# Kernel tuning notes

Hardware: AMD Instinct MI355X
Metric: run time of the kernel (lower is better)

The kernel has to match this reference:

```python
import jax, jax.numpy as jnp
import numpy as np

WAY = 100; SHOT = 5; QUERY = 100; DIM = 2048; K_VALUE = 512
NQ = WAY * QUERY  # 10000 query samples


def _l2norm(x, axis=-1):
    n = jnp.linalg.norm(x, axis=axis, keepdims=True)
    return x / jnp.maximum(n, 1e-12)  # matches F.normalize eps


def _compute_logits(feat, proto, temp):
    # feat [1,Q,D], proto [1,W,D] -> [1,Q,W]; 'dot' metric
    logits = jnp.einsum('bqd,bwd->bqw', feat, proto)
    norm = jnp.linalg.norm(logits, axis=1, keepdims=True)  # L2 over query dim, [1,1,W]
    return logits / (norm + 1e-6) * temp


def _proto_refine(logits, feat, proto, k_value):
    # vectorized version of the original Python loop with .item() scatter-adds
    abs_cert = jnp.max(logits, axis=2)[0]                 # [Q]
    k = min(abs_cert.shape[0], k_value)
    vals, idxs = jax.lax.top_k(abs_cert, k)               # [k]
    pseudo = jnp.argmax(logits[0, idxs], axis=1)          # [k] pseudo labels
    wf = (vals[:, None] * feat[0, idxs]) / k              # [k,D]
    add = jnp.zeros(proto.shape[1:], feat.dtype).at[pseudo].add(wf)  # [W,D]
    return proto + add


def _distance(shot, feat, temp_proto, way):
    proto = _l2norm(jnp.mean(shot, axis=-2))  # [1,W,D]
    feat = _l2norm(feat)                      # [1,Q,D]
    logits = _compute_logits(feat, proto, temp_proto)
    proto = _proto_refine(logits, feat, proto, K_VALUE)
    logits = _compute_logits(feat, proto, temp_proto)
    return logits.reshape(-1, way)[None]      # [1,Q,W]


def _distill_loss(logits_l, logits_h, weight):
    # faithful to F.log_softmax/softmax over dim=1 (query dim) and the
    # per-batch-row weighted KL sum in the original
    logp = jax.nn.log_softmax(logits_l, axis=1)
    p = jax.nn.softmax(logits_h, axis=1)
    kl = p * (jnp.log(p) - logp)              # [B,Q,W]
    wT = weight.T                             # [Q,B]
    summed = jnp.stack([jnp.sum(kl[i] * wT[i]) for i in range(logits_l.shape[0])])
    return jnp.mean(summed) / (jnp.sum(weight) + 1e-8)


def _certainties(shot, query, temp_proto, way):
    pk = _distance(shot, query, temp_proto, way)
    abs_c = jnp.max(pk, axis=2)                           # [1,Q]
    p = jax.nn.softmax(pk, axis=-1)
    rel_c = jnp.sum(p * jnp.log(p + 1e-10), axis=2)       # [1,Q]
    return abs_c, rel_c


def setup_inputs() -> dict:
    key = jax.random.key(0)
    k1, k2, k3, k4 = jax.random.split(key, 4)
    return {
        'x_shot': jax.random.normal(k1, (1, WAY, SHOT, DIM), jnp.float32),
        'x_query': jax.random.normal(k2, (1, NQ, DIM), jnp.float32),
        'dct_shot': jax.random.normal(k3, (1, WAY, SHOT, DIM), jnp.float32),
        'dct_query': jax.random.normal(k4, (1, NQ, DIM), jnp.float32),
        'temp_proto': jnp.float32(10.0),
        'temp': jnp.float32(1.0),
        'temp_dct': jnp.float32(1.0),
    }


def reference(x_shot, x_query, dct_shot, dct_query, temp_proto, temp, temp_dct):
    way = x_shot.shape[1]
    abs_c, rel_c = _certainties(x_shot, x_query, temp_proto, way)
    abs_cd, rel_cd = _certainties(dct_shot, dct_query, temp_proto, way)
    diff = np.asarray(abs_c - abs_cd + rel_c - rel_cd)[0]
    res_idx = np.where(diff > 0)[0]
    dct_idx = np.where(diff < 0)[0]
    zero = jnp.float32(0.0)
    if res_idx.size == 0 and dct_idx.size == 0:
        loss_dctl = zero; loss_resl = zero
    elif res_idx.size != 0 and dct_idx.size == 0:
        lrh = _distance(x_shot, x_query, temp_proto, way)
        ldl = _distance(dct_shot, dct_query, temp_proto, way)
        loss_dctl = _distill_loss(ldl, lrh, abs_c); loss_resl = zero
    elif res_idx.size == 0:
        ldh = _distance(dct_shot, dct_query, temp_proto, way)
        lrl = _distance(x_shot, x_query, temp_proto, way)
        loss_resl = _distill_loss(lrl, ldh, abs_cd); loss_dctl = zero
    else:
        lrh = _distance(x_shot, x_query[:, res_idx], temp_proto, way)
        ldl = _distance(dct_shot, dct_query[:, res_idx], temp_proto, way)
        ldh = _distance(dct_shot, dct_query[:, dct_idx], temp_proto, way)
        lrl = _distance(x_shot, x_query[:, dct_idx], temp_proto, way)
        loss_dctl = _distill_loss(ldl, lrh, abs_c[:, res_idx])
        loss_resl = _distill_loss(lrl, ldh, abs_cd[:, dct_idx])
    denom = jnp.maximum(abs_c + abs_cd, 1e-8)
    w_r = (abs_c / denom).T  # [Q,1]
    w_f = (abs_cd / denom).T
    return (temp * loss_resl, temp_dct * loss_dctl,
            jnp.asarray(res_idx), jnp.asarray(dct_idx), w_r, w_f)
```

## Files before the change

kernel.cpp:

```cpp
#include <hip/hip_runtime.h>
#include <cstdint>
#include <cstddef>

#define WAYS  100
#define SHOTS 5
#define NQ    10000
#define DIM   2048
#define KSEL  512

#define BQ 64
#define BW 64
#define BK 32
#define PAD 4
#define CQ 64

struct Ctrl {
  double klsum[2];
  double wsum[2];
  float  w0[2];
  int    R, Dn;
  unsigned int T[8];
  int rem[8];
  int kk[8];
};

__device__ __forceinline__ unsigned int monokey(float f){
  unsigned int b = __float_as_uint(f);
  return (b & 0x80000000u) ? ~b : (b | 0x80000000u);
}
__device__ __forceinline__ float dekey(unsigned int k){
  return (k & 0x80000000u) ? __uint_as_float(k & 0x7FFFFFFFu)
                           : __uint_as_float(~k);
}
__device__ __forceinline__ int decn(int sel, const Ctrl* c){
  return sel == 0 ? NQ : (sel == 1 ? c->R : c->Dn);
}

__global__ void proto_kernel(const float* __restrict__ xs, const float* __restrict__ dsh,
                             float* __restrict__ protoX, float* __restrict__ protoD){
  int b = blockIdx.x;
  const float* src = (b < WAYS) ? xs : dsh;
  float* dst = (b < WAYS) ? protoX : protoD;
  int w = (b < WAYS) ? b : b - WAYS;
  __shared__ float meanv[DIM];
  __shared__ float red[256];
  float loc = 0.f;
  for (int d = threadIdx.x; d < DIM; d += 256){
    float s = 0.f;
    for (int sh = 0; sh < SHOTS; sh++) s += src[((size_t)w*SHOTS + sh)*DIM + d];
    float m = s / (float)SHOTS;
    meanv[d] = m;
    loc += m*m;
  }
  red[threadIdx.x] = loc; __syncthreads();
  for (int st = 128; st > 0; st >>= 1){
    if (threadIdx.x < st) red[threadIdx.x] += red[threadIdx.x + st];
    __syncthreads();
  }
  float inv = 1.0f / fmaxf(sqrtf(red[0]), 1e-12f);
  for (int d = threadIdx.x; d < DIM; d += 256)
    dst[(size_t)w*DIM + d] = meanv[d] * inv;
}

__global__ __launch_bounds__(256)
void invnorm_kernel(const float* __restrict__ xq, const float* __restrict__ dq,
                    float* __restrict__ invnX, float* __restrict__ invnD){
  int row = blockIdx.x * 4 + (threadIdx.x >> 6);
  if (row >= 2*NQ) return;
  int lane = threadIdx.x & 63;
  const float* src = (row < NQ) ? xq : dq;
  float* dst = (row < NQ) ? invnX : invnD;
  int q = (row < NQ) ? row : row - NQ;
  const float4* r4 = (const float4*)(src + (size_t)q*DIM);
  float s = 0.f;
  for (int i = lane; i < DIM/4; i += 64){
    float4 v = r4[i];
    s += v.x*v.x + v.y*v.y + v.z*v.z + v.w*v.w;
  }
  for (int off = 32; off > 0; off >>= 1) s += __shfl_down(s, off);
  if (lane == 0) dst[q] = 1.0f / fmaxf(sqrtf(s), 1e-12f);
}

struct GemmArgs {
  const float* feat[4];
  const float* proto[4];
  const int*   idx[4];
  float*       outP[4];
  const float* invn[4];
  int          nSel[4];
  int          offSel[4];
  int          splitk;
  int          applyInvn;
  const Ctrl*  ctrl;
};

__global__ __launch_bounds__(256)
void gemm_batched(GemmArgs ga){
  int batch = blockIdx.z / ga.splitk;
  int s     = blockIdx.z % ga.splitk;
  int n = decn(ga.nSel[batch], ga.ctrl);
  int qBase = blockIdx.x * BQ;
  if (qBase >= n) return;
  int wBase = blockIdx.y * BW;
  int kLen  = DIM / ga.splitk;
  int kStart = s * kLen;

  __shared__ float As[BK][BQ+PAD];
  __shared__ float Bs[BK][BW+PAD];

  const float* feat  = ga.feat[batch];
  const float* proto = ga.proto[batch];
  const int*   idxl  = ga.idx[batch];

  int t = threadIdx.x;
  int lr = t & 63;
  int kv = t >> 6;
  int arow = qBase + lr;
  int garow = idxl ? idxl[min(arow, n-1)] : min(arow, n-1);
  const float* pA = feat + (size_t)garow*DIM + kStart + kv*4;
  int wrow = wBase + lr;
  bool bok = (wrow < WAYS);
  const float* pB = proto + (size_t)wrow*DIM + kStart + kv*4;

  int tx = t & 15, ty = t >> 4;
  float acc[4][4];
#pragma unroll
  for (int i = 0; i < 4; i++)
#pragma unroll
    for (int j = 0; j < 4; j++) acc[i][j] = 0.f;

  float4 av0, av1, bv0, bv1;
  const float4 z4 = make_float4(0.f,0.f,0.f,0.f);
  av0 = *(const float4*)pA;
  av1 = *(const float4*)(pA + 16);
  bv0 = bok ? *(const float4*)pB : z4;
  bv1 = bok ? *(const float4*)(pB + 16) : z4;

  for (int k0 = 0; k0 < kLen; k0 += BK){
    __syncthreads();
    int kk = kv*4;
    As[kk+0 ][lr]=av0.x; As[kk+1 ][lr]=av0.y; As[kk+2 ][lr]=av0.z; As[kk+3 ][lr]=av0.w;
    As[kk+16][lr]=av1.x; As[kk+17][lr]=av1.y; As[kk+18][lr]=av1.z; As[kk+19][lr]=av1.w;
    Bs[kk+0 ][lr]=bv0.x; Bs[kk+1 ][lr]=bv0.y; Bs[kk+2 ][lr]=bv0.z; Bs[kk+3 ][lr]=bv0.w;
    Bs[kk+16][lr]=bv1.x; Bs[kk+17][lr]=bv1.y; Bs[kk+18][lr]=bv1.z; Bs[kk+19][lr]=bv1.w;
    __syncthreads();
    if (k0 + BK < kLen){
      const float* qA = pA + k0 + BK;
      const float* qB = pB + k0 + BK;
      av0 = *(const float4*)qA; av1 = *(const float4*)(qA + 16);
      bv0 = bok ? *(const float4*)qB : z4;
      bv1 = bok ? *(const float4*)(qB + 16) : z4;
    }
#pragma unroll
    for (int kk2 = 0; kk2 < BK; kk2++){
      float4 a = *(const float4*)&As[kk2][ty*4];
      float4 b = *(const float4*)&Bs[kk2][tx*4];
      acc[0][0]+=a.x*b.x; acc[0][1]+=a.x*b.y; acc[0][2]+=a.x*b.z; acc[0][3]+=a.x*b.w;
      acc[1][0]+=a.y*b.x; acc[1][1]+=a.y*b.y; acc[1][2]+=a.y*b.z; acc[1][3]+=a.y*b.w;
      acc[2][0]+=a.z*b.x; acc[2][1]+=a.z*b.y; acc[2][2]+=a.z*b.z; acc[2][3]+=a.z*b.w;
      acc[3][0]+=a.w*b.x; acc[3][1]+=a.w*b.y; acc[3][2]+=a.w*b.z; acc[3][3]+=a.w*b.w;
    }
  }
  int rowOff = ga.offSel[batch] ? ga.ctrl->R : 0;
  float* outBase = ga.outP[batch] + ((size_t)s*NQ + (size_t)rowOff)*WAYS;
  int wc = wBase + tx*4;
#pragma unroll
  for (int i = 0; i < 4; i++){
    int q = qBase + ty*4 + i;
    if (q >= n) continue;
    float scr = 1.f;
    if (ga.applyInvn){
      int gq = idxl ? idxl[q] : q;
      scr = ga.invn[batch][gq];
    }
    float* dst = outBase + (size_t)q*WAYS + wc;
    if (wc + 3 < WAYS){
      *(float4*)dst = make_float4(acc[i][0]*scr, acc[i][1]*scr, acc[i][2]*scr, acc[i][3]*scr);
    } else {
#pragma unroll
      for (int j = 0; j < 4; j++) if (wc + j < WAYS) dst[j] = acc[i][j]*scr;
    }
  }
}

struct CombArgs {
  const float* P;
  const float* invn[2];
  float* Ltgt[2];
  double* colSq;
  int splitk;
};
__global__ __launch_bounds__(256)
void combine_batched(CombArgs ca){
  int b = blockIdx.y;
  int qBase = blockIdx.x * CQ;
  int t = threadIdx.x;
  int j = t % 25, r = t / 25;
  const float* Pb = ca.P + (size_t)b*ca.splitk*NQ*WAYS;
  const float* invn = ca.invn[b];
  float* L = ca.Ltgt[b];
  double sq0=0.0, sq1=0.0, sq2=0.0, sq3=0.0;
  if (r < 10){
    for (int i = r; i < CQ; i += 10){
      int q = qBase + i;
      if (q >= NQ) break;
      float sc = invn[q];
      const float* p0 = Pb + (size_t)q*WAYS + 4*j;
      float4 v = *(const float4*)p0;
      for (int s2 = 1; s2 < ca.splitk; s2++){
        float4 u = *(const float4*)(p0 + (size_t)s2*NQ*WAYS);
        v.x += u.x; v.y += u.y; v.z += u.z; v.w += u.w;
      }
      v.x *= sc; v.y *= sc; v.z *= sc; v.w *= sc;
      *(float4*)(L + (size_t)q*WAYS + 4*j) = v;
      sq0 += (double)v.x*(double)v.x;
      sq1 += (double)v.y*(double)v.y;
      sq2 += (double)v.z*(double)v.z;
      sq3 += (double)v.w*(double)v.w;
    }
  }
  __shared__ double red[WAYS][10];
  if (r < 10){
    red[4*j+0][r]=sq0; red[4*j+1][r]=sq1; red[4*j+2][r]=sq2; red[4*j+3][r]=sq3;
  }
  __syncthreads();
  if (t < WAYS){
    double s2 = 0.0;
#pragma unroll
    for (int rr = 0; rr < 10; rr++) s2 += red[t][rr];
    atomicAdd(ca.colSq + (size_t)b*WAYS + t, s2);
  }
}

struct StatArgs {
  const float* Lsrc[4];
  const int*   idx[4];
  int nSel[4];
  int offSel[4];
  double* colSq;
  unsigned* maxK;
  unsigned* negK;
  const Ctrl* ctrl;
};
__global__ __launch_bounds__(256)
void stats_batched(StatArgs sa){
  int b = blockIdx.y;
  int n = decn(sa.nSel[b], sa.ctrl);
  int qBase = blockIdx.x * CQ;
  if (qBase >= n) return;
  int t = threadIdx.x;
  int j = t % 25, r = t / 25;
  double sq0=0.0, sq1=0.0, sq2=0.0, sq3=0.0;
  float mx0=-3.4e38f,mx1=-3.4e38f,mx2=-3.4e38f,mx3=-3.4e38f;
  float mn0= 3.4e38f,mn1= 3.4e38f,mn2= 3.4e38f,mn3= 3.4e38f;
  if (r < 10){
    const int* idx = sa.idx[b];
    int rowOff = sa.offSel[b] ? sa.ctrl->R : 0;
    const float* L = sa.Lsrc[b] + (size_t)rowOff*WAYS;
    for (int i = r; i < CQ; i += 10){
      int q = qBase + i;
      if (q >= n) break;
      int gq = idx ? idx[q] : q;
      float4 v = *(const float4*)(L + (size_t)gq*WAYS + 4*j);
      sq0 += (double)v.x*(double)v.x; sq1 += (double)v.y*(double)v.y;
      sq2 += (double)v.z*(double)v.z; sq3 += (double)v.w*(double)v.w;
      mx0=fmaxf(mx0,v.x); mx1=fmaxf(mx1,v.y); mx2=fmaxf(mx2,v.z); mx3=fmaxf(mx3,v.w);
      mn0=fminf(mn0,v.x); mn1=fminf(mn1,v.y); mn2=fminf(mn2,v.z); mn3=fminf(mn3,v.w);
    }
  }
  __shared__ double red[WAYS][10];
  if (r < 10){
    red[4*j+0][r]=sq0; red[4*j+1][r]=sq1; red[4*j+2][r]=sq2; red[4*j+3][r]=sq3;
  }
  __syncthreads();
  if (t < WAYS){
    double s2 = 0.0;
#pragma unroll
    for (int rr = 0; rr < 10; rr++) s2 += red[t][rr];
    atomicAdd(sa.colSq + (size_t)b*WAYS + t, s2);
  }
  if (sa.maxK){
    __shared__ float redMx[WAYS][10], redMn[WAYS][10];
    if (r < 10){
      redMx[4*j+0][r]=mx0; redMx[4*j+1][r]=mx1; redMx[4*j+2][r]=mx2; redMx[4*j+3][r]=mx3;
      redMn[4*j+0][r]=mn0; redMn[4*j+1][r]=mn1; redMn[4*j+2][r]=mn2; redMn[4*j+3][r]=mn3;
    }
    __syncthreads();
    if (t < WAYS){
      float mx = -3.4e38f, mn = 3.4e38f;
#pragma unroll
      for (int rr = 0; rr < 10; rr++){ mx = fmaxf(mx, redMx[t][rr]); mn = fminf(mn, redMn[t][rr]); }
      atomicMax(sa.maxK + (size_t)b*WAYS + t, monokey(mx));
      atomicMax(sa.negK + (size_t)b*WAYS + t, monokey(-mn));
    }
  }
}

struct RS1Args {
  const float* Lsrc[4];
  const int*   idx[4];
  int nSel[4];
  const double* colSq;
  const float* tpP;
  const Ctrl* ctrl;
  float* absCert; unsigned* keys; int* pseudo;
};
__global__ __launch_bounds__(256)
void rowstats1_b(RS1Args a){
  int b = blockIdx.y;
  int n = decn(a.nSel[b], a.ctrl);
  __shared__ float sc[WAYS];
  int t = threadIdx.x;
  if (t < WAYS) sc[t] = (*a.tpP) / ((float)sqrt(a.colSq[(size_t)b*WAYS+t]) + 1e-6f);
  __syncthreads();
  int q = blockIdx.x*256 + t;
  if (q >= n) return;
  int gq = a.idx[b] ? a.idx[b][q] : q;
  const float* row = a.Lsrc[b] + (size_t)gq*WAYS;
  float m = row[0]*sc[0]; int am = 0;
  for (int w = 1; w < WAYS; w++){
    float v = row[w]*sc[w];
    if (v > m){ m = v; am = w; }
  }
  a.absCert[(size_t)b*NQ+q] = m;
  a.pseudo [(size_t)b*NQ+q] = am;
  a.keys   [(size_t)b*NQ+q] = monokey(m);
}

struct RS2Args {
  const float* Lsrc[2];
  const double* colSq;
  const float* tpP;
  float* absC; float* relC;
};
__global__ __launch_bounds__(256)
void rowstats2_b(RS2Args a){
  int b = blockIdx.y;
  __shared__ float sc[WAYS];
  int t = threadIdx.x;
  if (t < WAYS) sc[t] = (*a.tpP) / ((float)sqrt(a.colSq[(size_t)b*WAYS+t]) + 1e-6f);
  __syncthreads();
  int q = blockIdx.x*256 + t;
  if (q >= NQ) return;
  const float* row = a.Lsrc[b] + (size_t)q*WAYS;
  float m = row[0]*sc[0];
  for (int w = 1; w < WAYS; w++) m = fmaxf(m, row[w]*sc[w]);
  float s = 0.f;
  for (int w = 0; w < WAYS; w++) s += expf(row[w]*sc[w] - m);
  float inv = 1.0f / s, rel = 0.f;
  for (int w = 0; w < WAYS; w++){
    float p = expf(row[w]*sc[w] - m) * inv;
    rel += p * logf(p + 1e-10f);
  }
  a.absC[(size_t)b*NQ+q] = m;
  a.relC[(size_t)b*NQ+q] = rel;
}

struct SGArgs {
  const unsigned* keys; const float* absCert;
  int nSel[4]; int instBase;
  int* selIdx; float* selVal;
  Ctrl* ctrl;
};
__global__ __launch_bounds__(1024)
void selectgather_b(SGArgs a){
  int b = blockIdx.x;
  int inst = a.instBase + b;
  int n = decn(a.nSel[b], a.ctrl);
  int k = n < KSEL ? n : KSEL;
  const unsigned* keys = a.keys + (size_t)b*NQ;
  const float* absCert = a.absCert + (size_t)b*NQ;
  int* selIdx = a.selIdx + b*KSEL;
  float* selVal = a.selVal + b*KSEL;
  __shared__ int hist[256];
  __shared__ unsigned sprefix;
  __shared__ int srem;
  int t = threadIdx.x;
  if (t == 0){ sprefix = 0u; srem = k; }
  __syncthreads();
  int nv4 = n >> 2;
  for (int pass = 0; pass < 4; pass++){
    int shift = 24 - 8*pass;
    if (t < 256) hist[t] = 0;
    __syncthreads();
    unsigned pref = sprefix;
    unsigned mask = (pass == 0) ? 0u : (0xFFFFFFFFu << (shift + 8));
    for (int i = t; i < nv4; i += 1024){
      uint4 kv = ((const uint4*)keys)[i];
      if ((kv.x & mask) == pref) atomicAdd(&hist[(kv.x >> shift) & 255], 1);
      if ((kv.y & mask) == pref) atomicAdd(&hist[(kv.y >> shift) & 255], 1);
      if ((kv.z & mask) == pref) atomicAdd(&hist[(kv.z >> shift) & 255], 1);
      if ((kv.w & mask) == pref) atomicAdd(&hist[(kv.w >> shift) & 255], 1);
    }
    for (int i = 4*nv4 + t; i < n; i += 1024){
      unsigned key = keys[i];
      if ((key & mask) == pref) atomicAdd(&hist[(key >> shift) & 255], 1);
    }
    __syncthreads();
    if (t == 0){
      int acc = 0, rem = srem, sel = 0;
      for (int b2 = 255; b2 >= 0; b2--){
        int h = hist[b2];
        if (acc + h >= rem){ sel = b2; srem = rem - acc; break; }
        acc += h;
      }
      sprefix = pref | ((unsigned)sel << shift);
    }
    __syncthreads();
  }
  unsigned T = sprefix;
  int rem = srem;
  if (t == 0){ a.ctrl->T[inst] = T; a.ctrl->rem[inst] = rem; a.ctrl->kk[inst] = k; }
  int cntGT = k - rem;
  const int CH = 10;
  int q0 = t*CH;
  int fg[CH], fe[CH]; int cg = 0, ce = 0;
  for (int i = 0; i < CH; i++){
    int q = q0 + i; int g = 0, e = 0;
    if (q < n){ unsigned key = keys[q]; g = key > T; e = (key == T); }
    fg[i] = g; fe[i] = e; cg += g; ce += e;
  }
  __shared__ int sG[1024], sE[1024];
  sG[t] = cg; sE[t] = ce; __syncthreads();
  for (int s = 1; s < 1024; s <<= 1){
    int vg = t >= s ? sG[t-s] : 0;
    int ve = t >= s ? sE[t-s] : 0;
    __syncthreads();
    sG[t] += vg; sE[t] += ve;
    __syncthreads();
  }
  int posG = sG[t] - cg, posE = sE[t] - ce;
  for (int i = 0; i < CH; i++){
    int q = q0 + i;
    if (q >= n) break;
    if (fg[i]){ selIdx[posG] = q; selVal[posG] = absCert[q]; posG++; }
    else if (fe[i]){
      if (posE < rem){ selIdx[cntGT+posE] = q; selVal[cntGT+posE] = absCert[q]; }
      posE++;
    }
  }
}

struct RefArgs {
  const float* feat[4]; const int* idx[4];
  const float* invn[4]; const float* proto[4];
  const int* selIdx; const float* selVal;
  const int* pseudo;
  float* protoRef;
  int instBase;
  const Ctrl* ctrl;
};
__global__ __launch_bounds__(256)
void refine_b(RefArgs a){
  int b = blockIdx.y;
  int w = blockIdx.x;
  int k = a.ctrl->kk[a.instBase + b];
  const int* selIdx = a.selIdx + b*KSEL;
  const float* selVal = a.selVal + b*KSEL;
  const int* pseudo = a.pseudo + (size_t)b*NQ;
  const int* idxl = a.idx[b];
  __shared__ int   sRow[KSEL];
  __shared__ float sCoef[KSEL];
  int t = threadIdx.x;
  for (int j = t; j < k; j += 256){
    int srow = selIdx[j];
    int grow = idxl ? idxl[srow] : srow;
    sRow[j]  = (pseudo[srow] == w) ? grow : -1;
    sCoef[j] = selVal[j] * a.invn[b][grow] / (float)k;
  }
  __syncthreads();
  float4 acc0 = make_float4(0.f,0.f,0.f,0.f);
  float4 acc1 = make_float4(0.f,0.f,0.f,0.f);
  int d0 = t*4, d1 = t*4 + 1024;
  const float* feat = a.feat[b];
  for (int j = 0; j < k; j++){
    int grow = sRow[j];
    if (grow < 0) continue;
    float c = sCoef[j];
    const float* fr = feat + (size_t)grow*DIM;
    float4 f0 = *(const float4*)(fr + d0);
    float4 f1 = *(const float4*)(fr + d1);
    acc0.x += c*f0.x; acc0.y += c*f0.y; acc0.z += c*f0.z; acc0.w += c*f0.w;
    acc1.x += c*f1.x; acc1.y += c*f1.y; acc1.z += c*f1.z; acc1.w += c*f1.w;
  }
  const float* pw = a.proto[b] + (size_t)w*DIM;
  float* pr = a.protoRef + ((size_t)b*WAYS + w)*DIM;
  float4 p0 = *(const float4*)(pw + d0);
  float4 p1 = *(const float4*)(pw + d1);
  *(float4*)(pr + d0) = make_float4(p0.x+acc0.x, p0.y+acc0.y, p0.z+acc0.z, p0.w+acc0.w);
  *(float4*)(pr + d1) = make_float4(p1.x+acc1.x, p1.y+acc1.y, p1.z+acc1.z, p1.w+acc1.w);
}

__global__ __launch_bounds__(1024)
void diff_partition(const float* __restrict__ absC, const float* __restrict__ relC,
                    Ctrl* ctrl, int* __restrict__ resIdx, int* __restrict__ dctIdx,
                    float* __restrict__ out){
  const float* absCx = absC;        const float* absCd = absC + NQ;
  const float* relCx = relC;        const float* relCd = relC + NQ;
  const int CH = 10;
  int t = threadIdx.x, q0 = t*CH;
  int fr[CH], fd[CH]; int cr = 0, cd = 0;
  for (int i = 0; i < CH; i++){
    int q = q0 + i; int r = 0, dn = 0;
    if (q < NQ){
      float dv = absCx[q] - absCd[q] + relCx[q] - relCd[q];
      r = dv > 0.f; dn = dv < 0.f;
    }
    fr[i] = r; fd[i] = dn; cr += r; cd += dn;
  }
  __shared__ int sR[1024], sD[1024];
  sR[t] = cr; sD[t] = cd; __syncthreads();
  for (int s = 1; s < 1024; s <<= 1){
    int vr = t >= s ? sR[t-s] : 0;
    int vd = t >= s ? sD[t-s] : 0;
    __syncthreads();
    sR[t] += vr; sD[t] += vd;
    __syncthreads();
  }
  int R = sR[1023], Dn = sD[1023];
  int posR = sR[t] - cr, posD = sD[t] - cd;
  if (t == 0){ ctrl->R = R; ctrl->Dn = Dn; }
  for (int i = 0; i < CH; i++){
    int q = q0 + i;
    if (q >= NQ) break;
    if (fr[i]){ resIdx[posR] = q; out[2+posR] = (float)q; posR++; }
    if (fd[i]){ dctIdx[posD] = q; out[2+R+posD] = (float)q; posD++; }
  }
  for (int q = t; q < NQ; q += 1024){
    float a = absCx[q], b = absCd[q];
    float den = fmaxf(a + b, 1e-8f);
    out[2+R+Dn+q]      = a / den;
    out[2+R+Dn+NQ+q]   = b / den;
  }
}

struct SEArgs {
  const float* Lsrc[4];
  int nSel[4];
  int offSel[4];
  const double* colSq;
  const unsigned* maxK; const unsigned* negK;
  double* sumExp;
  const float* tpP;
  const Ctrl* ctrl;
};
__global__ __launch_bounds__(256)
void sumexp_batched(SEArgs a){
  int b = blockIdx.y;
  int n = decn(a.nSel[b], a.ctrl);
  int t = threadIdx.x;
  __shared__ float sc[WAYS], mv[WAYS];
  if (t < WAYS){
    float s = (*a.tpP) / ((float)sqrt(a.colSq[(size_t)b*WAYS+t]) + 1e-6f);
    float mxv = dekey(a.maxK[(size_t)b*WAYS+t]);
    float mnv = -dekey(a.negK[(size_t)b*WAYS+t]);
    sc[t] = s; mv[t] = (s >= 0.f) ? s*mxv : s*mnv;
  }
  __syncthreads();
  int qBase = blockIdx.x * CQ;
  if (qBase >= n) return;
  int j = t % 25, r = t / 25;
  double e0=0.0,e1=0.0,e2=0.0,e3=0.0;
  if (r < 10){
    int rowOff = a.offSel[b] ? a.ctrl->R : 0;
    const float* L = a.Lsrc[b] + (size_t)rowOff*WAYS;
    float s0=sc[4*j+0], s1=sc[4*j+1], s2=sc[4*j+2], s3=sc[4*j+3];
    float m0=mv[4*j+0], m1=mv[4*j+1], m2=mv[4*j+2], m3=mv[4*j+3];
    for (int i = r; i < CQ; i += 10){
      int q = qBase + i;
      if (q >= n) break;
      float4 v = *(const float4*)(L + (size_t)q*WAYS + 4*j);
      e0 += (double)expf(v.x*s0 - m0);
      e1 += (double)expf(v.y*s1 - m1);
      e2 += (double)expf(v.z*s2 - m2);
      e3 += (double)expf(v.w*s3 - m3);
    }
  }
  __shared__ double red[WAYS][10];
  if (r < 10){
    red[4*j+0][r]=e0; red[4*j+1][r]=e1; red[4*j+2][r]=e2; red[4*j+3][r]=e3;
  }
  __syncthreads();
  if (t < WAYS){
    double s2 = 0.0;
#pragma unroll
    for (int rr = 0; rr < 10; rr++) s2 += red[t][rr];
    atomicAdd(a.sumExp + (size_t)b*WAYS + t, s2);
  }
}

struct KLArgs {
  const float* bufs[4];
  int offSel[4];
  const double* colSq2;
  const unsigned* maxK; const unsigned* negK; const double* sumExp;
  const float* tpP;
  Ctrl* ctrl;
};
__global__ __launch_bounds__(256)
void klsum_batched(KLArgs a){
  int p = blockIdx.y;
  int bL = p ? 3 : 1, bH = p ? 2 : 0;
  int n = p ? a.ctrl->Dn : a.ctrl->R;
  __shared__ float scL[WAYS], lseL[WAYS], scH[WAYS], lseH[WAYS];
  int t = threadIdx.x;
  if (t < WAYS){
    float tp = *a.tpP;
    {
      float s = tp / ((float)sqrt(a.colSq2[(size_t)bL*WAYS+t]) + 1e-6f);
      float mxv = dekey(a.maxK[(size_t)bL*WAYS+t]);
      float mnv = -dekey(a.negK[(size_t)bL*WAYS+t]);
      float m = (s >= 0.f) ? s*mxv : s*mnv;
      scL[t] = s; lseL[t] = m + (float)log(a.sumExp[(size_t)bL*WAYS+t]);
    }
    {
      float s = tp / ((float)sqrt(a.colSq2[(size_t)bH*WAYS+t]) + 1e-6f);
      float mxv = dekey(a.maxK[(size_t)bH*WAYS+t]);
      float mnv = -dekey(a.negK[(size_t)bH*WAYS+t]);
      float m = (s >= 0.f) ? s*mxv : s*mnv;
      scH[t] = s; lseH[t] = m + (float)log(a.sumExp[(size_t)bH*WAYS+t]);
    }
  }
  __syncthreads();
  const float* Lm = a.bufs[bL] + (size_t)(a.offSel[bL] ? a.ctrl->R : 0)*WAYS;
  const float* Hm = a.bufs[bH] + (size_t)(a.offSel[bH] ? a.ctrl->R : 0)*WAYS;
  size_t total = (size_t)n * WAYS;
  double loc = 0.0;
  for (size_t i = (size_t)blockIdx.x*256 + t; i < total; i += (size_t)gridDim.x*256){
    int w = (int)(i % WAYS);
    float lh = Hm[i]*scH[w] - lseH[w];
    float ll = Lm[i]*scL[w] - lseL[w];
    loc += (double)(expf(lh) * (lh - ll));
  }
  __shared__ double sd[256];
  sd[t] = loc; __syncthreads();
  for (int st = 128; st > 0; st >>= 1){
    if (t < st) sd[t] += sd[t + st];
    __syncthreads();
  }
  if (t == 0) atomicAdd(&a.ctrl->klsum[p], sd[0]);
}

__global__ __launch_bounds__(256)
void wsum_b(const float* __restrict__ absC, const int* __restrict__ resIdx,
            const int* __restrict__ dctIdx, Ctrl* ctrl){
  int b = blockIdx.y;
  int n = b ? ctrl->Dn : ctrl->R;
  const float* src = b ? (absC + NQ) : absC;
  const int* idx = b ? dctIdx : resIdx;
  double loc = 0.0;
  for (int i = blockIdx.x*256 + threadIdx.x; i < n; i += gridDim.x*256)
    loc += (double)src[idx[i]];
  __shared__ double sd[256];
  sd[threadIdx.x] = loc; __syncthreads();
  for (int st = 128; st > 0; st >>= 1){
    if (threadIdx.x < st) sd[threadIdx.x] += sd[threadIdx.x + st];
    __syncthreads();
  }
  if (threadIdx.x == 0) atomicAdd(&ctrl->wsum[b], sd[0]);
  if (blockIdx.x == 0 && threadIdx.x == 0 && n > 0) ctrl->w0[b] = src[idx[0]];
}

__global__ void final_kernel(const Ctrl* ctrl, const float* tP, const float* tdP,
                             float* out){
  if (threadIdx.x == 0 && blockIdx.x == 0){
    float lossd = ctrl->w0[0] * (float)ctrl->klsum[0] / ((float)ctrl->wsum[0] + 1e-8f);
    float lossr = ctrl->w0[1] * (float)ctrl->klsum[1] / ((float)ctrl->wsum[1] + 1e-8f);
    out[0] = (*tP)  * lossr;
    out[1] = (*tdP) * lossd;
  }
}

extern "C" void kernel_launch(void* const* d_in, const int* in_sizes, int n_in,
                              void* d_out, int out_size, void* d_ws, size_t ws_size,
                              hipStream_t stream)
{
  const float* xs  = (const float*)d_in[0];
  const float* xq  = (const float*)d_in[1];
  const float* dsh = (const float*)d_in[2];
  const float* dq  = (const float*)d_in[3];
  const float* tpP = (const float*)d_in[4];
  const float* tP  = (const float*)d_in[5];
  const float* tdP = (const float*)d_in[6];
  float* out = (float*)d_out;

  char* base = (char*)d_ws;
  Ctrl* ctrl = (Ctrl*)base;
  double*   colSqAll = (double*)(base + 512);
  unsigned* maxK     = (unsigned*)(base + 512 + 9600);
  unsigned* negK     = maxK + 4*WAYS;
  double*   sumExp   = (double*)(base + 512 + 9600 + 3200);
  size_t zone = 512 + 9600 + 3200 + 3200;
  size_t off = (zone + 255) & ~(size_t)255;
  auto alloc = [&](size_t nElem)->void*{ void* p = base + off; off += nElem*4; return p; };
  float* protoX   = (float*)alloc((size_t)WAYS*DIM);
  float* protoD   = (float*)alloc((size_t)WAYS*DIM);
  float* protoRef = (float*)alloc((size_t)4*WAYS*DIM);
  float* invnX    = (float*)alloc(NQ);
  float* invnD    = (float*)alloc(NQ);
  float* Lx0      = (float*)alloc((size_t)NQ*WAYS);
  float* Ld0      = (float*)alloc((size_t)NQ*WAYS);
  float* absCertF = (float*)alloc((size_t)2*NQ);
  unsigned* keysF = (unsigned*)alloc((size_t)2*NQ);
  int*   pseudoF  = (int*)alloc((size_t)2*NQ);
  float* absCertS = (float*)alloc((size_t)4*NQ);
  unsigned* keysS = (unsigned*)alloc((size_t)4*NQ);
  int*   pseudoS  = (int*)alloc((size_t)4*NQ);
  float* absC     = (float*)alloc((size_t)2*NQ);
  float* relC     = (float*)alloc((size_t)2*NQ);
  int*   selIdx   = (int*)alloc((size_t)4*KSEL);
  float* selVal   = (float*)alloc((size_t)4*KSEL);
  int*   resIdx   = (int*)alloc(NQ);
  int*   dctIdx   = (int*)alloc(NQ);

  float* P = (float*)(base + ((off + 255) & ~(size_t)255));
  size_t offP = (off + 255) & ~(size_t)255;
  int splitkF;
  if (offP + (size_t)2*2*NQ*WAYS*4 <= ws_size) splitkF = 2;
  else if (offP + (size_t)2*1*NQ*WAYS*4 <= ws_size) splitkF = 1;
  else return;
  float* Pb0 = P;
  float* Pb1 = P + (size_t)splitkF*NQ*WAYS;
  float* LxF = Pb0;
  float* LdF = Pb1;

  hipMemsetAsync(base, 0, zone, stream);
  proto_kernel<<<2*WAYS, 256, 0, stream>>>(xs, dsh, protoX, protoD);
  invnorm_kernel<<<(2*NQ+3)/4, 256, 0, stream>>>(xq, dq, invnX, invnD);

  dim3 gFull((NQ + BQ - 1)/BQ, (WAYS + BW - 1)/BW, 2*splitkF);
  int sgrid = (NQ + CQ - 1)/CQ;

  GemmArgs g1{};
  g1.feat[0]=xq; g1.feat[1]=dq;
  g1.proto[0]=protoX; g1.proto[1]=protoD;
  g1.nSel[0]=0; g1.nSel[1]=0;
  g1.splitk=splitkF; g1.ctrl=ctrl;
  if (splitkF > 1){
    g1.outP[0]=Pb0; g1.outP[1]=Pb1; g1.applyInvn=0;
  } else {
    g1.outP[0]=Lx0; g1.outP[1]=Ld0; g1.applyInvn=1;
    g1.invn[0]=invnX; g1.invn[1]=invnD;
  }
  gemm_batched<<<gFull,256,0,stream>>>(g1);
  if (splitkF > 1){
    CombArgs c1{}; c1.P=P; c1.invn[0]=invnX; c1.invn[1]=invnD;
    c1.Ltgt[0]=Lx0; c1.Ltgt[1]=Ld0; c1.colSq=colSqAll; c1.splitk=splitkF;
    combine_batched<<<dim3(sgrid,2),256,0,stream>>>(c1);
  } else {
    StatArgs s1{}; s1.Lsrc[0]=Lx0; s1.Lsrc[1]=Ld0;
    s1.nSel[0]=0; s1.nSel[1]=0; s1.colSq=colSqAll; s1.ctrl=ctrl;
    stats_batched<<<dim3(sgrid,2),256,0,stream>>>(s1);
  }
  RS1Args r1{}; r1.Lsrc[0]=Lx0; r1.Lsrc[1]=Ld0;
  r1.nSel[0]=0; r1.nSel[1]=0; r1.colSq=colSqAll; r1.tpP=tpP; r1.ctrl=ctrl;
  r1.absCert=absCertF; r1.keys=keysF; r1.pseudo=pseudoF;
  rowstats1_b<<<dim3((NQ+255)/256,2),256,0,stream>>>(r1);
  SGArgs sg1{}; sg1.keys=keysF; sg1.absCert=absCertF;
  sg1.nSel[0]=0; sg1.nSel[1]=0; sg1.instBase=0;
  sg1.selIdx=selIdx; sg1.selVal=selVal; sg1.ctrl=ctrl;
  selectgather_b<<<2,1024,0,stream>>>(sg1);
  RefArgs rf1{}; rf1.feat[0]=xq; rf1.feat[1]=dq;
  rf1.invn[0]=invnX; rf1.invn[1]=invnD;
  rf1.proto[0]=protoX; rf1.proto[1]=protoD;
  rf1.selIdx=selIdx; rf1.selVal=selVal; rf1.pseudo=pseudoF;
  rf1.protoRef=protoRef; rf1.instBase=0; rf1.ctrl=ctrl;
  refine_b<<<dim3(WAYS,2),256,0,stream>>>(rf1);

  GemmArgs g2 = g1;
  g2.proto[0]=protoRef; g2.proto[1]=protoRef + (size_t)WAYS*DIM;
  if (splitkF == 1){ g2.outP[0]=LxF; g2.outP[1]=LdF; }
  gemm_batched<<<gFull,256,0,stream>>>(g2);
  if (splitkF > 1){
    CombArgs c2{}; c2.P=P; c2.invn[0]=invnX; c2.invn[1]=invnD;
    c2.Ltgt[0]=LxF; c2.Ltgt[1]=LdF; c2.colSq=colSqAll + 2*WAYS; c2.splitk=splitkF;
    combine_batched<<<dim3(sgrid,2),256,0,stream>>>(c2);
  } else {
    StatArgs s2{}; s2.Lsrc[0]=LxF; s2.Lsrc[1]=LdF;
    s2.nSel[0]=0; s2.nSel[1]=0; s2.colSq=colSqAll + 2*WAYS; s2.ctrl=ctrl;
    stats_batched<<<dim3(sgrid,2),256,0,stream>>>(s2);
  }
  RS2Args r2{}; r2.Lsrc[0]=LxF; r2.Lsrc[1]=LdF;
  r2.colSq=colSqAll + 2*WAYS; r2.tpP=tpP; r2.absC=absC; r2.relC=relC;
  rowstats2_b<<<dim3((NQ+255)/256,2),256,0,stream>>>(r2);

  diff_partition<<<1,1024,0,stream>>>(absC, relC, ctrl, resIdx, dctIdx, out);

  StatArgs ss1{};
  ss1.Lsrc[0]=Lx0; ss1.Lsrc[1]=Ld0; ss1.Lsrc[2]=Ld0; ss1.Lsrc[3]=Lx0;
  ss1.idx[0]=resIdx; ss1.idx[1]=resIdx; ss1.idx[2]=dctIdx; ss1.idx[3]=dctIdx;
  ss1.nSel[0]=1; ss1.nSel[1]=1; ss1.nSel[2]=2; ss1.nSel[3]=2;
  ss1.colSq=colSqAll + 4*WAYS; ss1.ctrl=ctrl;
  stats_batched<<<dim3(sgrid,4),256,0,stream>>>(ss1);
  RS1Args rs{}; rs.Lsrc[0]=Lx0; rs.Lsrc[1]=Ld0; rs.Lsrc[2]=Ld0; rs.Lsrc[3]=Lx0;
  rs.idx[0]=resIdx; rs.idx[1]=resIdx; rs.idx[2]=dctIdx; rs.idx[3]=dctIdx;
  rs.nSel[0]=1; rs.nSel[1]=1; rs.nSel[2]=2; rs.nSel[3]=2;
  rs.colSq=colSqAll + 4*WAYS; rs.tpP=tpP; rs.ctrl=ctrl;
  rs.absCert=absCertS; rs.keys=keysS; rs.pseudo=pseudoS;
  rowstats1_b<<<dim3((NQ+255)/256,4),256,0,stream>>>(rs);
  SGArgs sg2{}; sg2.keys=keysS; sg2.absCert=absCertS;
  sg2.nSel[0]=1; sg2.nSel[1]=1; sg2.nSel[2]=2; sg2.nSel[3]=2; sg2.instBase=2;
  sg2.selIdx=selIdx; sg2.selVal=selVal; sg2.ctrl=ctrl;
  selectgather_b<<<4,1024,0,stream>>>(sg2);
  RefArgs rf2{};
  rf2.feat[0]=xq; rf2.feat[1]=dq; rf2.feat[2]=dq; rf2.feat[3]=xq;
  rf2.idx[0]=resIdx; rf2.idx[1]=resIdx; rf2.idx[2]=dctIdx; rf2.idx[3]=dctIdx;
  rf2.invn[0]=invnX; rf2.invn[1]=invnD; rf2.invn[2]=invnD; rf2.invn[3]=invnX;
  rf2.proto[0]=protoX; rf2.proto[1]=protoD; rf2.proto[2]=protoD; rf2.proto[3]=protoX;
  rf2.selIdx=selIdx; rf2.selVal=selVal; rf2.pseudo=pseudoS;
  rf2.protoRef=protoRef; rf2.instBase=2; rf2.ctrl=ctrl;
  refine_b<<<dim3(WAYS,4),256,0,stream>>>(rf2);
  GemmArgs gs{};
  gs.feat[0]=xq; gs.feat[1]=dq; gs.feat[2]=dq; gs.feat[3]=xq;
  gs.proto[0]=protoRef;
  gs.proto[1]=protoRef + (size_t)WAYS*DIM;
  gs.proto[2]=protoRef + (size_t)2*WAYS*DIM;
  gs.proto[3]=protoRef + (size_t)3*WAYS*DIM;
  gs.outP[0]=Pb0; gs.outP[1]=Pb1; gs.outP[2]=Pb1; gs.outP[3]=Pb0;
  gs.offSel[0]=0; gs.offSel[1]=0; gs.offSel[2]=1; gs.offSel[3]=1;
  gs.idx[0]=resIdx; gs.idx[1]=resIdx; gs.idx[2]=dctIdx; gs.idx[3]=dctIdx;
  gs.invn[0]=invnX; gs.invn[1]=invnD; gs.invn[2]=invnD; gs.invn[3]=invnX;
  gs.nSel[0]=1; gs.nSel[1]=1; gs.nSel[2]=2; gs.nSel[3]=2;
  gs.splitk=1; gs.applyInvn=1; gs.ctrl=ctrl;
  gemm_batched<<<dim3((NQ+BQ-1)/BQ,(WAYS+BW-1)/BW,4),256,0,stream>>>(gs);
  StatArgs ss2{};
  ss2.Lsrc[0]=Pb0; ss2.Lsrc[1]=Pb1; ss2.Lsrc[2]=Pb1; ss2.Lsrc[3]=Pb0;
  ss2.offSel[0]=0; ss2.offSel[1]=0; ss2.offSel[2]=1; ss2.offSel[3]=1;
  ss2.nSel[0]=1; ss2.nSel[1]=1; ss2.nSel[2]=2; ss2.nSel[3]=2;
  ss2.colSq=colSqAll + 8*WAYS; ss2.maxK=maxK; ss2.negK=negK; ss2.ctrl=ctrl;
  stats_batched<<<dim3(sgrid,4),256,0,stream>>>(ss2);
  SEArgs se{};
  se.Lsrc[0]=Pb0; se.Lsrc[1]=Pb1; se.Lsrc[2]=Pb1; se.Lsrc[3]=Pb0;
  se.offSel[0]=0; se.offSel[1]=0; se.offSel[2]=1; se.offSel[3]=1;
  se.nSel[0]=1; se.nSel[1]=1; se.nSel[2]=2; se.nSel[3]=2;
  se.colSq=colSqAll + 8*WAYS; se.maxK=maxK; se.negK=negK;
  se.sumExp=sumExp; se.tpP=tpP; se.ctrl=ctrl;
  sumexp_batched<<<dim3(sgrid,4),256,0,stream>>>(se);
  KLArgs kl{};
  kl.bufs[0]=Pb0; kl.bufs[1]=Pb1; kl.bufs[2]=Pb1; kl.bufs[3]=Pb0;
  kl.offSel[0]=0; kl.offSel[1]=0; kl.offSel[2]=1; kl.offSel[3]=1;
  kl.colSq2=colSqAll + 8*WAYS; kl.maxK=maxK; kl.negK=negK; kl.sumExp=sumExp;
  kl.tpP=tpP; kl.ctrl=ctrl;
  klsum_batched<<<dim3(64,2),256,0,stream>>>(kl);
  wsum_b<<<dim3((NQ+255)/256,2),256,0,stream>>>(absC, resIdx, dctIdx, ctrl);
  final_kernel<<<1,64,0,stream>>>(ctrl, tP, tdP, out);
}
```

Measured before the change: 1.106 ms.

## Enlarge GEMM query tile to 128 and add split-K for subset GEMMs

Doubles the GEMM query tile to 128 rows, so each thread computes an 8x4 micro-tile. This raises arithmetic intensity per shared-memory load and halves the number of prototype tile reloads. It also allows split-K of 4 when the workspace fits, and applies split-K to the second-stage subset GEMMs, with a new combine kernel that sums the partials and applies the inverse norms. The larger tile uses more registers and may lower occupancy, and split-K adds extra partial-buffer traffic plus one more kernel launch.

```diff
diff --git a/kernel.cpp b/kernel.cpp
--- a/kernel.cpp
+++ b/kernel.cpp
@@ -8,7 +8,7 @@
 #define DIM   2048
 #define KSEL  512
 
-#define BQ 64
+#define BQ 128
 #define BW 64
 #define BK 32
 #define PAD 4
@@ -113,60 +113,72 @@
   const int*   idxl  = ga.idx[batch];
 
   int t = threadIdx.x;
-  int lr = t & 63;
-  int kv = t >> 6;
-  int arow = qBase + lr;
+  int qr = t & 127;
+  int akk0 = t >> 7;
+  int arow = qBase + qr;
   int garow = idxl ? idxl[min(arow, n-1)] : min(arow, n-1);
-  const float* pA = feat + (size_t)garow*DIM + kStart + kv*4;
-  int wrow = wBase + lr;
+  const float* pA = feat + (size_t)garow*DIM + kStart;
+
+  int wr = t & 63;
+  int wrow = wBase + wr;
   bool bok = (wrow < WAYS);
-  const float* pB = proto + (size_t)wrow*DIM + kStart + kv*4;
+  const float* pB = proto + (size_t)wrow*DIM + kStart;
+  int bkk0 = t >> 6;
 
   int tx = t & 15, ty = t >> 4;
-  float acc[4][4];
-#pragma unroll
-  for (int i = 0; i < 4; i++)
+  float acc[8][4];
+#pragma unroll
+  for (int i = 0; i < 8; i++)
 #pragma unroll
     for (int j = 0; j < 4; j++) acc[i][j] = 0.f;
 
-  float4 av0, av1, bv0, bv1;
+  float4 av[4], bv[2];
   const float4 z4 = make_float4(0.f,0.f,0.f,0.f);
-  av0 = *(const float4*)pA;
-  av1 = *(const float4*)(pA + 16);
-  bv0 = bok ? *(const float4*)pB : z4;
-  bv1 = bok ? *(const float4*)(pB + 16) : z4;
+#pragma unroll
+  for (int i = 0; i < 4; i++) av[i] = *(const float4*)(pA + (akk0 + 2*i)*4);
+#pragma unroll
+  for (int i = 0; i < 2; i++)
+    bv[i] = bok ? *(const float4*)(pB + (bkk0 + 4*i)*4) : z4;
 
   for (int k0 = 0; k0 < kLen; k0 += BK){
     __syncthreads();
-    int kk = kv*4;
-    As[kk+0 ][lr]=av0.x; As[kk+1 ][lr]=av0.y; As[kk+2 ][lr]=av0.z; As[kk+3 ][lr]=av0.w;
-    As[kk+16][lr]=av1.x; As[kk+17][lr]=av1.y; As[kk+18][lr]=av1.z; As[kk+19][lr]=av1.w;
-    Bs[kk+0 ][lr]=bv0.x; Bs[kk+1 ][lr]=bv0.y; Bs[kk+2 ][lr]=bv0.z; Bs[kk+3 ][lr]=bv0.w;
-    Bs[kk+16][lr]=bv1.x; Bs[kk+17][lr]=bv1.y; Bs[kk+18][lr]=bv1.z; Bs[kk+19][lr]=bv1.w;
+#pragma unroll
+    for (int i = 0; i < 4; i++){
+      int kk = (akk0 + 2*i)*4;
+      As[kk+0][qr]=av[i].x; As[kk+1][qr]=av[i].y; As[kk+2][qr]=av[i].z; As[kk+3][qr]=av[i].w;
+    }
+#pragma unroll
+    for (int i = 0; i < 2; i++){
+      int kk = (bkk0 + 4*i)*4;
+      Bs[kk+0][wr]=bv[i].x; Bs[kk+1][wr]=bv[i].y; Bs[kk+2][wr]=bv[i].z; Bs[kk+3][wr]=bv[i].w;
+    }
     __syncthreads();
     if (k0 + BK < kLen){
-      const float* qA = pA + k0 + BK;
-      const float* qB = pB + k0 + BK;
-      av0 = *(const float4*)qA; av1 = *(const float4*)(qA + 16);
-      bv0 = bok ? *(const float4*)qB : z4;
-      bv1 = bok ? *(const float4*)(qB + 16) : z4;
+#pragma unroll
+      for (int i = 0; i < 4; i++) av[i] = *(const float4*)(pA + k0 + BK + (akk0 + 2*i)*4);
+#pragma unroll
+      for (int i = 0; i < 2; i++)
+        bv[i] = bok ? *(const float4*)(pB + k0 + BK + (bkk0 + 4*i)*4) : z4;
     }
 #pragma unroll
     for (int kk2 = 0; kk2 < BK; kk2++){
-      float4 a = *(const float4*)&As[kk2][ty*4];
-      float4 b = *(const float4*)&Bs[kk2][tx*4];
-      acc[0][0]+=a.x*b.x; acc[0][1]+=a.x*b.y; acc[0][2]+=a.x*b.z; acc[0][3]+=a.x*b.w;
-      acc[1][0]+=a.y*b.x; acc[1][1]+=a.y*b.y; acc[1][2]+=a.y*b.z; acc[1][3]+=a.y*b.w;
-      acc[2][0]+=a.z*b.x; acc[2][1]+=a.z*b.y; acc[2][2]+=a.z*b.z; acc[2][3]+=a.z*b.w;
-      acc[3][0]+=a.w*b.x; acc[3][1]+=a.w*b.y; acc[3][2]+=a.w*b.z; acc[3][3]+=a.w*b.w;
+      float4 a0 = *(const float4*)&As[kk2][ty*8];
+      float4 a1 = *(const float4*)&As[kk2][ty*8+4];
+      float4 b  = *(const float4*)&Bs[kk2][tx*4];
+      float a8[8] = {a0.x,a0.y,a0.z,a0.w,a1.x,a1.y,a1.z,a1.w};
+#pragma unroll
+      for (int i = 0; i < 8; i++){
+        acc[i][0]+=a8[i]*b.x; acc[i][1]+=a8[i]*b.y;
+        acc[i][2]+=a8[i]*b.z; acc[i][3]+=a8[i]*b.w;
+      }
     }
   }
   int rowOff = ga.offSel[batch] ? ga.ctrl->R : 0;
   float* outBase = ga.outP[batch] + ((size_t)s*NQ + (size_t)rowOff)*WAYS;
   int wc = wBase + tx*4;
 #pragma unroll
-  for (int i = 0; i < 4; i++){
-    int q = qBase + ty*4 + i;
+  for (int i = 0; i < 8; i++){
+    int q = qBase + ty*8 + i;
     if (q >= n) continue;
     float scr = 1.f;
     if (ga.applyInvn){
@@ -229,6 +241,41 @@
 #pragma unroll
     for (int rr = 0; rr < 10; rr++) s2 += red[t][rr];
     atomicAdd(ca.colSq + (size_t)b*WAYS + t, s2);
+  }
+}
+
+struct CombSubArgs {
+  float* buf[2];
+  const float* invn[2];
+  const int* resIdx; const int* dctIdx;
+  int splitk;
+  const Ctrl* ctrl;
+};
+__global__ __launch_bounds__(256)
+void combine_sub(CombSubArgs a){
+  int bfi = blockIdx.y;
+  int R = a.ctrl->R, Dn = a.ctrl->Dn;
+  int n = R + Dn;
+  int qBase = blockIdx.x * CQ;
+  if (qBase >= n) return;
+  int t = threadIdx.x;
+  int j = t % 25, r = t / 25;
+  if (r >= 10) return;
+  float* B = a.buf[bfi];
+  const float* invn = a.invn[bfi];
+  for (int i = r; i < CQ; i += 10){
+    int q = qBase + i;
+    if (q >= n) break;
+    int gq = (q < R) ? a.resIdx[q] : a.dctIdx[q - R];
+    float sc = invn[gq];
+    float* p0 = B + (size_t)q*WAYS + 4*j;
+    float4 v = *(const float4*)p0;
+    for (int s2 = 1; s2 < a.splitk; s2++){
+      float4 u = *(const float4*)(p0 + (size_t)s2*NQ*WAYS);
+      v.x += u.x; v.y += u.y; v.z += u.z; v.w += u.w;
+    }
+    v.x *= sc; v.y *= sc; v.z *= sc; v.w *= sc;
+    *(float4*)p0 = v;
   }
 }
 
@@ -713,10 +760,11 @@
   int*   resIdx   = (int*)alloc(NQ);
   int*   dctIdx   = (int*)alloc(NQ);
 
-  float* P = (float*)(base + ((off + 255) & ~(size_t)255));
   size_t offP = (off + 255) & ~(size_t)255;
+  float* P = (float*)(base + offP);
   int splitkF;
-  if (offP + (size_t)2*2*NQ*WAYS*4 <= ws_size) splitkF = 2;
+  if      (offP + (size_t)2*4*NQ*WAYS*4 <= ws_size) splitkF = 4;
+  else if (offP + (size_t)2*2*NQ*WAYS*4 <= ws_size) splitkF = 2;
   else if (offP + (size_t)2*1*NQ*WAYS*4 <= ws_size) splitkF = 1;
   else return;
   float* Pb0 = P;
@@ -810,6 +858,8 @@
   rf2.selIdx=selIdx; rf2.selVal=selVal; rf2.pseudo=pseudoS;
   rf2.protoRef=protoRef; rf2.instBase=2; rf2.ctrl=ctrl;
   refine_b<<<dim3(WAYS,4),256,0,stream>>>(rf2);
+
+  int splitkS = splitkF;
   GemmArgs gs{};
   gs.feat[0]=xq; gs.feat[1]=dq; gs.feat[2]=dq; gs.feat[3]=xq;
   gs.proto[0]=protoRef;
@@ -821,8 +871,16 @@
   gs.idx[0]=resIdx; gs.idx[1]=resIdx; gs.idx[2]=dctIdx; gs.idx[3]=dctIdx;
   gs.invn[0]=invnX; gs.invn[1]=invnD; gs.invn[2]=invnD; gs.invn[3]=invnX;
   gs.nSel[0]=1; gs.nSel[1]=1; gs.nSel[2]=2; gs.nSel[3]=2;
-  gs.splitk=1; gs.applyInvn=1; gs.ctrl=ctrl;
-  gemm_batched<<<dim3((NQ+BQ-1)/BQ,(WAYS+BW-1)/BW,4),256,0,stream>>>(gs);
+  gs.splitk=splitkS; gs.applyInvn=(splitkS == 1); gs.ctrl=ctrl;
+  gemm_batched<<<dim3((NQ+BQ-1)/BQ,(WAYS+BW-1)/BW,4*splitkS),256,0,stream>>>(gs);
+  if (splitkS > 1){
+    CombSubArgs cs{};
+    cs.buf[0]=Pb0; cs.buf[1]=Pb1;
+    cs.invn[0]=invnX; cs.invn[1]=invnD;
+    cs.resIdx=resIdx; cs.dctIdx=dctIdx;
+    cs.splitk=splitkS; cs.ctrl=ctrl;
+    combine_sub<<<dim3(sgrid,2),256,0,stream>>>(cs);
+  }
   StatArgs ss2{};
   ss2.Lsrc[0]=Pb0; ss2.Lsrc[1]=Pb1; ss2.Lsrc[2]=Pb1; ss2.Lsrc[3]=Pb0;
   ss2.offSel[0]=0; ss2.offSel[1]=0; ss2.offSel[2]=1; ss2.offSel[3]=1;
```

After: 950.4 us. 1.16x faster.
